# Performance work log

Measured on AMD Instinct MI355X. Metric: run time of the kernel, lower is better.

Reference implementation:

```python
import jax, jax.numpy as jnp
import numpy as np

N0, N1, N2 = 200000, 100000, 50000
D = 16          # sampled neighbor fan-out
DIM = 128       # input_dim == hidden dims


def setup_inputs() -> dict:
    key = jax.random.key(0)
    ks = jax.random.split(key, 9)
    return {
        "features": jax.random.normal(ks[0], (N0, DIM), jnp.float32),
        "W1": jax.random.normal(ks[1], (2 * DIM, DIM), jnp.float32) * 0.02,
        "b1": jnp.zeros((DIM,), jnp.float32),
        "W2": jax.random.normal(ks[2], (2 * DIM, DIM), jnp.float32) * 0.02,
        "b2": jnp.zeros((DIM,), jnp.float32),
        "neigh1_idx": jax.random.randint(ks[3], (N1, D), 0, N0, jnp.int32),
        "self1_idx": jax.random.randint(ks[4], (N1,), 0, N0, jnp.int32),
        "neigh2_idx": jax.random.randint(ks[5], (N2, D), 0, N1, jnp.int32),
        "self2_idx": jax.random.randint(ks[6], (N2,), 0, N1, jnp.int32),
    }


def _sage_layer(h_prev, self_idx, neigh_idx, W, b):
    # mean-aggregate sampled neighbors: gather [n, D, d] -> mean over D
    neigh = jnp.mean(h_prev[neigh_idx], axis=1)          # [n, d]
    x = jnp.concatenate([h_prev[self_idx], neigh], axis=-1)  # [n, 2d]
    return jax.nn.relu(x @ W + b)                        # [n, d_out]


def reference(features, W1, b1, W2, b2, neigh1_idx, self1_idx, neigh2_idx, self2_idx):
    h1 = _sage_layer(features, self1_idx, neigh1_idx, W1, b1)  # [N1, DIM]
    h2 = _sage_layer(h1, self2_idx, neigh2_idx, W2, b2)        # [N2, DIM]
    return h2
```

## Files before the change

kernel.cpp:

```cpp
#include <hip/hip_runtime.h>
#include <hip/hip_bf16.h>

typedef __attribute__((ext_vector_type(8))) short bf16x8;
typedef __attribute__((ext_vector_type(4))) float f32x4;

#define DIM   128
#define KD    256
#define FAN   16
#define TILE  32
#define XS_STRIDE 264
#define WP_LAYER_SHORTS (8*8*64*8)
#define PERSIST_BLOCKS 1536

__device__ __forceinline__ unsigned short f2bf(float f) {
    __hip_bfloat16 h = __float2bfloat16(f);
    return *reinterpret_cast<unsigned short*>(&h);
}
__device__ __forceinline__ float bflo(unsigned int u) { return __uint_as_float(u << 16); }
__device__ __forceinline__ float bfhi(unsigned int u) { return __uint_as_float(u & 0xffff0000u); }

__global__ __launch_bounds__(256)
void cvt_bf16_kernel(const float* __restrict__ in, uint2* __restrict__ out, int n4)
{
    const int stride = gridDim.x * blockDim.x;
    for (int i = blockIdx.x * blockDim.x + threadIdx.x; i < n4; i += stride) {
        const float4 v = reinterpret_cast<const float4*>(in)[i];
        uint2 o;
        o.x = (unsigned int)f2bf(v.x) | ((unsigned int)f2bf(v.y) << 16);
        o.y = (unsigned int)f2bf(v.z) | ((unsigned int)f2bf(v.w) << 16);
        out[i] = o;
    }
}

__global__ __launch_bounds__(256)
void wpack_kernel(const float* __restrict__ W1, const float* __restrict__ W2,
                  unsigned short* __restrict__ wp)
{
    const int b = blockIdx.x;
    const float* W = (b & 8) ? W2 : W1;
    unsigned short* dst = wp + ((b & 8) ? WP_LAYER_SHORTS : 0);
    const int t   = b & 7;
    const int tid = threadIdx.x;
    const int lane = tid & 63, wid = tid >> 6;
    const int l15 = lane & 15, lg = lane >> 4;
    #pragma unroll
    for (int s = 0; s < 2; ++s) {
        const int ks = wid + s * 4;
        bf16x8 v;
        #pragma unroll
        for (int j = 0; j < 8; ++j)
            v[j] = (short)f2bf(W[(size_t)(ks * 32 + lg * 8 + j) * DIM + t * 16 + l15]);
        *reinterpret_cast<bf16x8*>(dst + ((size_t)(t * 8 + ks) * 64 + lane) * 8) = v;
    }
}

template<bool SRC_BF, bool DST_BF>
__global__ __launch_bounds__(256, 6)
void sage_layer(const void* __restrict__ src,
                const unsigned short* __restrict__ wp,
                const float* __restrict__ bias,
                const int*  __restrict__ nidx,
                const int*  __restrict__ sidx,
                void* __restrict__ dst,
                int nnodes, int ntiles)
{
    __shared__ unsigned short xs[TILE * XS_STRIDE];

    const int tid  = threadIdx.x;
    const int lane = tid & 63;
    const int wid  = tid >> 6;
    const int l15  = lane & 15;
    const int lg   = lane >> 4;

    float bv[2];
    bv[0] = bias[(2 * wid + 0) * 16 + l15];
    bv[1] = bias[(2 * wid + 1) * 16 + l15];

    for (int tile = blockIdx.x; tile < ntiles; tile += gridDim.x) {
        const int nb = tile * TILE;
        __syncthreads();

        #pragma unroll 4
        for (int i = 0; i < 8; ++i) {
            int n = nb + wid * 8 + i;
            if (n >= nnodes) n = nnodes - 1;
            const int sn = sidx[n];
            const int* nn = nidx + (size_t)n * FAN;
            unsigned int su;
            float ax = 0.f, ay = 0.f;
            if (SRC_BF) {
                const unsigned int* srcu = (const unsigned int*)src;
                su = srcu[(size_t)sn * 64 + lane];
                #pragma unroll
                for (int j = 0; j < FAN; ++j) {
                    const unsigned int u = srcu[(size_t)nn[j] * 64 + lane];
                    ax += bflo(u); ay += bfhi(u);
                }
            } else {
                const float* srcf = (const float*)src;
                const float2 sv = *reinterpret_cast<const float2*>(srcf + (size_t)sn * DIM + 2 * lane);
                su = (unsigned int)f2bf(sv.x) | ((unsigned int)f2bf(sv.y) << 16);
                #pragma unroll
                for (int j = 0; j < FAN; ++j) {
                    const float2 v = *reinterpret_cast<const float2*>(srcf + (size_t)nn[j] * DIM + 2 * lane);
                    ax += v.x; ay += v.y;
                }
            }
            ax *= 0.0625f; ay *= 0.0625f;
            const unsigned int mu = (unsigned int)f2bf(ax) | ((unsigned int)f2bf(ay) << 16);
            unsigned int* row = reinterpret_cast<unsigned int*>(xs + (size_t)(wid * 8 + i) * XS_STRIDE);
            row[lane]      = su;
            row[64 + lane] = mu;
        }
        __syncthreads();

        int woff = 0;
        asm volatile("" : "+v"(woff));
        const unsigned short* wpt = wp + woff;

        f32x4 acc[2][2];
        #pragma unroll
        for (int mt = 0; mt < 2; ++mt)
            #pragma unroll
            for (int t = 0; t < 2; ++t)
                acc[mt][t] = (f32x4){0.f, 0.f, 0.f, 0.f};

        const int tg0 = 2 * wid, tg1 = 2 * wid + 1;
        #pragma unroll
        for (int ks = 0; ks < 8; ++ks) {
            const bf16x8 af0 = *reinterpret_cast<const bf16x8*>(
                xs + (size_t)(l15) * XS_STRIDE + ks * 32 + lg * 8);
            const bf16x8 af1 = *reinterpret_cast<const bf16x8*>(
                xs + (size_t)(16 + l15) * XS_STRIDE + ks * 32 + lg * 8);
            const bf16x8 w0 = *reinterpret_cast<const bf16x8*>(
                wpt + ((size_t)(tg0 * 8 + ks) * 64 + lane) * 8);
            const bf16x8 w1 = *reinterpret_cast<const bf16x8*>(
                wpt + ((size_t)(tg1 * 8 + ks) * 64 + lane) * 8);
            acc[0][0] = __builtin_amdgcn_mfma_f32_16x16x32_bf16(af0, w0, acc[0][0], 0, 0, 0);
            acc[1][0] = __builtin_amdgcn_mfma_f32_16x16x32_bf16(af1, w0, acc[1][0], 0, 0, 0);
            acc[0][1] = __builtin_amdgcn_mfma_f32_16x16x32_bf16(af0, w1, acc[0][1], 0, 0, 0);
            acc[1][1] = __builtin_amdgcn_mfma_f32_16x16x32_bf16(af1, w1, acc[1][1], 0, 0, 0);
        }

        #pragma unroll
        for (int mt = 0; mt < 2; ++mt) {
            #pragma unroll
            for (int t = 0; t < 2; ++t) {
                const int col = (2 * wid + t) * 16 + l15;
                #pragma unroll
                for (int r = 0; r < 4; ++r) {
                    const int n = nb + mt * 16 + lg * 4 + r;
                    if (n < nnodes) {
                        const float v = acc[mt][t][r] + bv[t];
                        const float rv = v > 0.f ? v : 0.f;
                        if (DST_BF)
                            ((unsigned short*)dst)[(size_t)n * DIM + col] = f2bf(rv);
                        else
                            ((float*)dst)[(size_t)n * DIM + col] = rv;
                    }
                }
            }
        }
    }
}

extern "C" void kernel_launch(void* const* d_in, const int* in_sizes, int n_in,
                              void* d_out, int out_size, void* d_ws, size_t ws_size,
                              hipStream_t stream)
{
    const float* features = (const float*)d_in[0];
    const float* W1       = (const float*)d_in[1];
    const float* b1       = (const float*)d_in[2];
    const float* W2       = (const float*)d_in[3];
    const float* b2       = (const float*)d_in[4];
    const int*   n1idx    = (const int*)d_in[5];
    const int*   s1idx    = (const int*)d_in[6];
    const int*   n2idx    = (const int*)d_in[7];
    const int*   s2idx    = (const int*)d_in[8];

    const int NF = in_sizes[0];
    const int N1 = in_sizes[6];
    const int N2 = in_sizes[8];

    const size_t fbf_bytes = (size_t)NF * 2;
    const size_t h1_bytes  = (size_t)N1 * DIM * 2;
    const size_t wp_bytes  = (size_t)2 * WP_LAYER_SHORTS * 2;
    const bool full = ws_size >= fbf_bytes + h1_bytes + wp_bytes;

    unsigned char* ws = (unsigned char*)d_ws;
    unsigned short* fbf = nullptr;
    unsigned short* h1  = nullptr;
    unsigned short* wpk = nullptr;
    if (full) {
        fbf = (unsigned short*)ws;
        h1  = (unsigned short*)(ws + fbf_bytes);
        wpk = (unsigned short*)(ws + fbf_bytes + h1_bytes);
    } else {
        h1  = (unsigned short*)ws;
        wpk = (unsigned short*)(ws + h1_bytes);
    }

    wpack_kernel<<<16, 256, 0, stream>>>(W1, W2, wpk);
    if (full)
        cvt_bf16_kernel<<<2048, 256, 0, stream>>>(features, (uint2*)fbf, NF / 4);

    const int t1 = (N1 + TILE - 1) / TILE;
    const int t2 = (N2 + TILE - 1) / TILE;
    const int g1 = t1 < PERSIST_BLOCKS ? t1 : PERSIST_BLOCKS;
    const int g2 = t2 < PERSIST_BLOCKS ? t2 : PERSIST_BLOCKS;

    if (full)
        sage_layer<true,  true><<<g1, 256, 0, stream>>>(fbf, wpk, b1, n1idx, s1idx, h1, N1, t1);
    else
        sage_layer<false, true><<<g1, 256, 0, stream>>>(features, wpk, b1, n1idx, s1idx, h1, N1, t1);

    sage_layer<true, false><<<g2, 256, 0, stream>>>(h1, wpk + WP_LAYER_SHORTS, b2,
                                                    n2idx, s2idx, (float*)d_out, N2, t2);
}
```

Measured before the change: 340.5 us.

## Vectorize bf16 neighbor gather with 16-byte loads and drop persistent loop

The bf16 gather path now assigns 16 lanes per node, so each lane loads 16 bytes per neighbor row and a wave processes four nodes at once. Neighbor and self indices are first loaded coalesced into shared memory. The persistent tile loop is replaced by one block per tile, and the bias is read in the epilogue. The aim is more memory-level parallelism and fewer load instructions in the gather, at the cost of more blocks launched and per-wave LDS index staging without explicit barriers.

```diff
diff --git a/kernel.cpp b/kernel.cpp
--- a/kernel.cpp
+++ b/kernel.cpp
@@ -10,7 +10,6 @@
 #define TILE  32
 #define XS_STRIDE 264
 #define WP_LAYER_SHORTS (8*8*64*8)
-#define PERSIST_BLOCKS 1536
 
 __device__ __forceinline__ unsigned short f2bf(float f) {
     __hip_bfloat16 h = __float2bfloat16(f);
@@ -62,49 +61,72 @@
                 const int*  __restrict__ nidx,
                 const int*  __restrict__ sidx,
                 void* __restrict__ dst,
-                int nnodes, int ntiles)
-{
-    __shared__ unsigned short xs[TILE * XS_STRIDE];
+                int nnodes)
+{
+    __shared__ __align__(16) unsigned short xs[TILE * XS_STRIDE];
+    __shared__ int nib[4][72];
 
     const int tid  = threadIdx.x;
     const int lane = tid & 63;
     const int wid  = tid >> 6;
     const int l15  = lane & 15;
     const int lg   = lane >> 4;
-
-    float bv[2];
-    bv[0] = bias[(2 * wid + 0) * 16 + l15];
-    bv[1] = bias[(2 * wid + 1) * 16 + l15];
-
-    for (int tile = blockIdx.x; tile < ntiles; tile += gridDim.x) {
-        const int nb = tile * TILE;
-        __syncthreads();
-
+    const int nb   = blockIdx.x * TILE;
+
+    if (SRC_BF) {
+        const int g = lg;
+        const int s = l15;
+        const uint4* srcv = (const uint4*)src;
+
+        #pragma unroll 1
+        for (int it = 0; it < 2; ++it) {
+            const int nbase = nb + wid * 8 + it * 4;
+            {
+                int n = nbase + g; if (n >= nnodes) n = nnodes - 1;
+                nib[wid][g * 17 + s] = nidx[(size_t)n * FAN + s];
+                if (lane < 4) {
+                    int n2 = nbase + lane; if (n2 >= nnodes) n2 = nnodes - 1;
+                    nib[wid][68 + lane] = sidx[n2];
+                }
+            }
+            const int sn = nib[wid][68 + g];
+            const uint4 sv = srcv[(size_t)sn * 16 + s];
+            float a0 = 0.f, a1 = 0.f, a2 = 0.f, a3 = 0.f;
+            float a4 = 0.f, a5 = 0.f, a6 = 0.f, a7 = 0.f;
+            #pragma unroll
+            for (int j = 0; j < FAN; ++j) {
+                const int nj = nib[wid][g * 17 + j];
+                const uint4 v = srcv[(size_t)nj * 16 + s];
+                a0 += bflo(v.x); a1 += bfhi(v.x);
+                a2 += bflo(v.y); a3 += bfhi(v.y);
+                a4 += bflo(v.z); a5 += bfhi(v.z);
+                a6 += bflo(v.w); a7 += bfhi(v.w);
+            }
+            uint4 mv;
+            mv.x = (unsigned int)f2bf(a0 * 0.0625f) | ((unsigned int)f2bf(a1 * 0.0625f) << 16);
+            mv.y = (unsigned int)f2bf(a2 * 0.0625f) | ((unsigned int)f2bf(a3 * 0.0625f) << 16);
+            mv.z = (unsigned int)f2bf(a4 * 0.0625f) | ((unsigned int)f2bf(a5 * 0.0625f) << 16);
+            mv.w = (unsigned int)f2bf(a6 * 0.0625f) | ((unsigned int)f2bf(a7 * 0.0625f) << 16);
+            const int ln = wid * 8 + it * 4 + g;
+            uint4* rowp = reinterpret_cast<uint4*>(xs + (size_t)ln * XS_STRIDE);
+            rowp[s]      = sv;
+            rowp[16 + s] = mv;
+        }
+    } else {
         #pragma unroll 4
         for (int i = 0; i < 8; ++i) {
             int n = nb + wid * 8 + i;
             if (n >= nnodes) n = nnodes - 1;
             const int sn = sidx[n];
             const int* nn = nidx + (size_t)n * FAN;
-            unsigned int su;
+            const float* srcf = (const float*)src;
+            const float2 sv = *reinterpret_cast<const float2*>(srcf + (size_t)sn * DIM + 2 * lane);
+            unsigned int su = (unsigned int)f2bf(sv.x) | ((unsigned int)f2bf(sv.y) << 16);
             float ax = 0.f, ay = 0.f;
-            if (SRC_BF) {
-                const unsigned int* srcu = (const unsigned int*)src;
-                su = srcu[(size_t)sn * 64 + lane];
-                #pragma unroll
-                for (int j = 0; j < FAN; ++j) {
-                    const unsigned int u = srcu[(size_t)nn[j] * 64 + lane];
-                    ax += bflo(u); ay += bfhi(u);
-                }
-            } else {
-                const float* srcf = (const float*)src;
-                const float2 sv = *reinterpret_cast<const float2*>(srcf + (size_t)sn * DIM + 2 * lane);
-                su = (unsigned int)f2bf(sv.x) | ((unsigned int)f2bf(sv.y) << 16);
-                #pragma unroll
-                for (int j = 0; j < FAN; ++j) {
-                    const float2 v = *reinterpret_cast<const float2*>(srcf + (size_t)nn[j] * DIM + 2 * lane);
-                    ax += v.x; ay += v.y;
-                }
+            #pragma unroll
+            for (int j = 0; j < FAN; ++j) {
+                const float2 v = *reinterpret_cast<const float2*>(srcf + (size_t)nn[j] * DIM + 2 * lane);
+                ax += v.x; ay += v.y;
             }
             ax *= 0.0625f; ay *= 0.0625f;
             const unsigned int mu = (unsigned int)f2bf(ax) | ((unsigned int)f2bf(ay) << 16);
@@ -112,52 +134,53 @@
             row[lane]      = su;
             row[64 + lane] = mu;
         }
-        __syncthreads();
-
-        int woff = 0;
-        asm volatile("" : "+v"(woff));
-        const unsigned short* wpt = wp + woff;
-
-        f32x4 acc[2][2];
+    }
+    __syncthreads();
+
+    int woff = 0;
+    asm volatile("" : "+v"(woff));
+    const unsigned short* wpt = wp + woff;
+
+    f32x4 acc[2][2];
+    #pragma unroll
+    for (int mt = 0; mt < 2; ++mt)
         #pragma unroll
-        for (int mt = 0; mt < 2; ++mt)
+        for (int t = 0; t < 2; ++t)
+            acc[mt][t] = (f32x4){0.f, 0.f, 0.f, 0.f};
+
+    const int tg0 = 2 * wid, tg1 = 2 * wid + 1;
+    #pragma unroll
+    for (int ks = 0; ks < 8; ++ks) {
+        const bf16x8 af0 = *reinterpret_cast<const bf16x8*>(
+            xs + (size_t)(l15) * XS_STRIDE + ks * 32 + lg * 8);
+        const bf16x8 af1 = *reinterpret_cast<const bf16x8*>(
+            xs + (size_t)(16 + l15) * XS_STRIDE + ks * 32 + lg * 8);
+        const bf16x8 w0 = *reinterpret_cast<const bf16x8*>(
+            wpt + ((size_t)(tg0 * 8 + ks) * 64 + lane) * 8);
+        const bf16x8 w1 = *reinterpret_cast<const bf16x8*>(
+            wpt + ((size_t)(tg1 * 8 + ks) * 64 + lane) * 8);
+        acc[0][0] = __builtin_amdgcn_mfma_f32_16x16x32_bf16(af0, w0, acc[0][0], 0, 0, 0);
+        acc[1][0] = __builtin_amdgcn_mfma_f32_16x16x32_bf16(af1, w0, acc[1][0], 0, 0, 0);
+        acc[0][1] = __builtin_amdgcn_mfma_f32_16x16x32_bf16(af0, w1, acc[0][1], 0, 0, 0);
+        acc[1][1] = __builtin_amdgcn_mfma_f32_16x16x32_bf16(af1, w1, acc[1][1], 0, 0, 0);
+    }
+
+    #pragma unroll
+    for (int mt = 0; mt < 2; ++mt) {
+        #pragma unroll
+        for (int t = 0; t < 2; ++t) {
+            const int col = (2 * wid + t) * 16 + l15;
+            const float bvt = bias[col];
             #pragma unroll
-            for (int t = 0; t < 2; ++t)
-                acc[mt][t] = (f32x4){0.f, 0.f, 0.f, 0.f};
-
-        const int tg0 = 2 * wid, tg1 = 2 * wid + 1;
-        #pragma unroll
-        for (int ks = 0; ks < 8; ++ks) {
-            const bf16x8 af0 = *reinterpret_cast<const bf16x8*>(
-                xs + (size_t)(l15) * XS_STRIDE + ks * 32 + lg * 8);
-            const bf16x8 af1 = *reinterpret_cast<const bf16x8*>(
-                xs + (size_t)(16 + l15) * XS_STRIDE + ks * 32 + lg * 8);
-            const bf16x8 w0 = *reinterpret_cast<const bf16x8*>(
-                wpt + ((size_t)(tg0 * 8 + ks) * 64 + lane) * 8);
-            const bf16x8 w1 = *reinterpret_cast<const bf16x8*>(
-                wpt + ((size_t)(tg1 * 8 + ks) * 64 + lane) * 8);
-            acc[0][0] = __builtin_amdgcn_mfma_f32_16x16x32_bf16(af0, w0, acc[0][0], 0, 0, 0);
-            acc[1][0] = __builtin_amdgcn_mfma_f32_16x16x32_bf16(af1, w0, acc[1][0], 0, 0, 0);
-            acc[0][1] = __builtin_amdgcn_mfma_f32_16x16x32_bf16(af0, w1, acc[0][1], 0, 0, 0);
-            acc[1][1] = __builtin_amdgcn_mfma_f32_16x16x32_bf16(af1, w1, acc[1][1], 0, 0, 0);
-        }
-
-        #pragma unroll
-        for (int mt = 0; mt < 2; ++mt) {
-            #pragma unroll
-            for (int t = 0; t < 2; ++t) {
-                const int col = (2 * wid + t) * 16 + l15;
-                #pragma unroll
-                for (int r = 0; r < 4; ++r) {
-                    const int n = nb + mt * 16 + lg * 4 + r;
-                    if (n < nnodes) {
-                        const float v = acc[mt][t][r] + bv[t];
-                        const float rv = v > 0.f ? v : 0.f;
-                        if (DST_BF)
-                            ((unsigned short*)dst)[(size_t)n * DIM + col] = f2bf(rv);
-                        else
-                            ((float*)dst)[(size_t)n * DIM + col] = rv;
-                    }
+            for (int r = 0; r < 4; ++r) {
+                const int n = nb + mt * 16 + lg * 4 + r;
+                if (n < nnodes) {
+                    const float v = acc[mt][t][r] + bvt;
+                    const float rv = v > 0.f ? v : 0.f;
+                    if (DST_BF)
+                        ((unsigned short*)dst)[(size_t)n * DIM + col] = f2bf(rv);
+                    else
+                        ((float*)dst)[(size_t)n * DIM + col] = rv;
                 }
             }
         }
@@ -206,14 +229,12 @@
 
     const int t1 = (N1 + TILE - 1) / TILE;
     const int t2 = (N2 + TILE - 1) / TILE;
-    const int g1 = t1 < PERSIST_BLOCKS ? t1 : PERSIST_BLOCKS;
-    const int g2 = t2 < PERSIST_BLOCKS ? t2 : PERSIST_BLOCKS;
 
     if (full)
-        sage_layer<true,  true><<<g1, 256, 0, stream>>>(fbf, wpk, b1, n1idx, s1idx, h1, N1, t1);
+        sage_layer<true,  true><<<t1, 256, 0, stream>>>(fbf, wpk, b1, n1idx, s1idx, h1, N1);
     else
-        sage_layer<false, true><<<g1, 256, 0, stream>>>(features, wpk, b1, n1idx, s1idx, h1, N1, t1);
-
-    sage_layer<true, false><<<g2, 256, 0, stream>>>(h1, wpk + WP_LAYER_SHORTS, b2,
-                                                    n2idx, s2idx, (float*)d_out, N2, t2);
-}
+        sage_layer<false, true><<<t1, 256, 0, stream>>>(features, wpk, b1, n1idx, s1idx, h1, N1);
+
+    sage_layer<true, false><<<t2, 256, 0, stream>>>(h1, wpk + WP_LAYER_SHORTS, b2,
+                                                    n2idx, s2idx, (float*)d_out, N2);
+}
```

New measurement: 284.4 us. 1.2x faster.
